# Optimization experiments

Measured on AMD Instinct MI355X. Metric: run time of the kernel, lower is better.

The kernel has to match this reference:

```python
import jax, jax.numpy as jnp
import numpy as np

TEMPERATURE = 1.0
EPS = 1e-12  # matches torch F.normalize eps


def setup_inputs() -> dict:
    key = jax.random.key(0)
    k1, k2 = jax.random.split(key)
    query_features = jax.random.normal(k1, (128, 640, 32, 32), dtype=jnp.float32)
    support_features = jax.random.normal(k2, (5, 640, 32, 32), dtype=jnp.float32)
    return {"query_features": query_features, "support_features": support_features}


def _l2norm(x):
    # F.normalize: x / max(||x||, eps)
    n = jnp.linalg.norm(x, axis=-1, keepdims=True)
    return x / jnp.maximum(n, EPS)


def reference(query_features, support_features):
    NQ, C, H, W = query_features.shape
    # (NQ, C, H, W) -> (NQ, N, C)
    q_patches = query_features.reshape(NQ, C, H * W).transpose(0, 2, 1)
    s_patches = support_features.reshape(support_features.shape[0], C, H * W).transpose(0, 2, 1)
    s_proto = s_patches.mean(axis=0)          # (N, C) prototype over shots
    q_norm = _l2norm(q_patches)               # (NQ, N, C)
    s_norm = _l2norm(s_proto)                 # (N, C)
    sim = jnp.einsum('qnc,mc->qnm', q_norm, s_norm)  # (NQ, N, N)
    max_sim = sim.max(axis=-1)                # (NQ, N) best support patch per query patch
    scores = max_sim.mean(axis=-1) / TEMPERATURE  # (NQ,)
    return scores
```

## Files before the change

### kernel.cpp

```cpp
#include <hip/hip_runtime.h>
#include <stdint.h>


#define NQ   128
#define NP   1024
#define C    640
#define NSH  5
#define EPSN 1e-12f
#define QPITCH 132

typedef __attribute__((ext_vector_type(8))) __bf16 bf16x8;
typedef __attribute__((ext_vector_type(4))) float  f32x4;
typedef __attribute__((ext_vector_type(4))) unsigned int u32x4;

__device__ __forceinline__ unsigned short f2bf(float f) {
  unsigned int u = __builtin_bit_cast(unsigned int, f);
  unsigned int r = (u + 0x7fffu + ((u >> 16) & 1u)) >> 16;
  return (unsigned short)r;
}

__device__ __forceinline__ void gload16(const void* g, void* l) {
  __builtin_amdgcn_global_load_lds(
      (const __attribute__((address_space(1))) void*)g,
      (__attribute__((address_space(3))) void*)l, 16, 0, 0);
}

__global__ __launch_bounds__(256) void prep_s_kernel(
    const float* __restrict__ sup, unsigned short* __restrict__ Sb) {
  __shared__ float red[16][17];
  __shared__ float invn[16];
  int t = threadIdx.x;
  int tm = t & 15, tcg = t >> 4;
  int m = blockIdx.x * 16 + tm;

  float sumsq = 0.f;
  for (int c = tcg; c < C; c += 16) {
    float p = 0.f;
    #pragma unroll
    for (int s = 0; s < NSH; ++s) p += sup[((size_t)s * C + c) * NP + m];
    p *= 0.2f;
    sumsq += p * p;
  }
  red[tcg][tm] = sumsq;
  __syncthreads();
  if (t < 16) {
    float s = 0.f;
    #pragma unroll
    for (int g = 0; g < 16; ++g) s += red[g][t];
    invn[t] = 1.f / fmaxf(sqrtf(s), EPSN);
  }
  __syncthreads();
  float iv = invn[tm];
  for (int c = tcg; c < C; c += 16) {
    float p = 0.f;
    #pragma unroll
    for (int s = 0; s < NSH; ++s) p += sup[((size_t)s * C + c) * NP + m];
    p *= 0.2f;
    Sb[((size_t)(c >> 3) * 1024 + m) * 8 + (c & 7)] = f2bf(p * iv);
  }
}

template <int CC>
__device__ __forceinline__ void q_step(const float* __restrict__ Qbase,
                                       float* __restrict__ qchunk,
                                       f32x4& sq, int nq, int cg, int arow,
                                       int quad,
                                       bf16x8& f00, bf16x8& f01,
                                       bf16x8& f10, bf16x8& f11) {
  #pragma unroll
  for (int i = 0; i < 8; ++i) {
    int c = cg + i * 8;
    f32x4 v = *(const f32x4*)(Qbase + (size_t)(CC * 64 + c) * NP);
    sq += v * v;
    *(f32x4*)&qchunk[c * QPITCH + nq * 4] = v;
  }
  __syncthreads();
  #pragma unroll
  for (int s = 0; s < 2; ++s) {
    #pragma unroll
    for (int nf = 0; nf < 2; ++nf) {
      int row = arow + nf * 16;
      unsigned int uw[4];
      #pragma unroll
      for (int jj = 0; jj < 4; ++jj) {
        int k0 = s * 32 + quad * 8 + jj * 2;
        float v0 = qchunk[k0 * QPITCH + row];
        float v1 = qchunk[(k0 + 1) * QPITCH + row];
        uw[jj] = (unsigned)f2bf(v0) | ((unsigned)f2bf(v1) << 16);
      }
      u32x4 uu = {uw[0], uw[1], uw[2], uw[3]};
      bf16x8 r = __builtin_bit_cast(bf16x8, uu);
      if (s == 0 && nf == 0) f00 = r;
      else if (s == 0 && nf == 1) f01 = r;
      else if (s == 1 && nf == 0) f10 = r;
      else f11 = r;
    }
  }
  __syncthreads();
}

__global__ __launch_bounds__(256, 2) void fused_gemm_kernel(
    const float* __restrict__ Q, const unsigned short* __restrict__ Sb,
    float* __restrict__ partial) {
  __shared__ __align__(16) char Rg[40960];
  __shared__ float invq[128];
  __shared__ float maxbuf[128];
  __shared__ float ssum[2];

  const int t = threadIdx.x;
  const int lane = t & 63, w = t >> 6;
  const int l15 = lane & 15, quad = lane >> 4;
  const int q = blockIdx.x, ns = blockIdx.y;
  const int n0 = ns * 128;

  float* qchunk = (float*)Rg;
  float* qsums  = (float*)(Rg + 33792);
  bf16x8 aF[40];
  const int nq = t & 31, cg = t >> 5;
  const float* Qbase = Q + (size_t)q * C * NP + n0 + nq * 4;
  const int arow = w * 32 + l15;
  f32x4 sq = {0.f, 0.f, 0.f, 0.f};

  q_step<0>(Qbase, qchunk, sq, nq, cg, arow, quad, aF[0],  aF[1],  aF[2],  aF[3]);
  q_step<1>(Qbase, qchunk, sq, nq, cg, arow, quad, aF[4],  aF[5],  aF[6],  aF[7]);
  q_step<2>(Qbase, qchunk, sq, nq, cg, arow, quad, aF[8],  aF[9],  aF[10], aF[11]);
  q_step<3>(Qbase, qchunk, sq, nq, cg, arow, quad, aF[12], aF[13], aF[14], aF[15]);
  q_step<4>(Qbase, qchunk, sq, nq, cg, arow, quad, aF[16], aF[17], aF[18], aF[19]);
  q_step<5>(Qbase, qchunk, sq, nq, cg, arow, quad, aF[20], aF[21], aF[22], aF[23]);
  q_step<6>(Qbase, qchunk, sq, nq, cg, arow, quad, aF[24], aF[25], aF[26], aF[27]);
  q_step<7>(Qbase, qchunk, sq, nq, cg, arow, quad, aF[28], aF[29], aF[30], aF[31]);
  q_step<8>(Qbase, qchunk, sq, nq, cg, arow, quad, aF[32], aF[33], aF[34], aF[35]);
  q_step<9>(Qbase, qchunk, sq, nq, cg, arow, quad, aF[36], aF[37], aF[38], aF[39]);

  #pragma unroll
  for (int j = 0; j < 4; ++j) qsums[cg * 128 + nq * 4 + j] = sq[j];
  __syncthreads();
  if (t < 128) {
    float s = 0.f;
    #pragma unroll
    for (int g = 0; g < 8; ++g) s += qsums[g * 128 + t];
    invq[t] = 1.f / fmaxf(sqrtf(s), EPSN);
  }
  __syncthreads();

  unsigned short* Ss = (unsigned short*)Rg;
  f32x4 ninf = {-3.0e38f, -3.0e38f, -3.0e38f, -3.0e38f};
  f32x4 rm[2] = {ninf, ninf};

  for (int mt = 0; mt < 16; ++mt) {
    f32x4 zero = {0.f, 0.f, 0.f, 0.f};
    f32x4 acc[2][4];
    #pragma unroll
    for (int nf = 0; nf < 2; ++nf)
      #pragma unroll
      for (int mf = 0; mf < 4; ++mf) acc[nf][mf] = zero;

    #pragma unroll
    for (int h = 0; h < 2; ++h) {
      const unsigned short* gsrc =
          Sb + ((size_t)(h * 40 + w) * 1024 + mt * 64 + lane) * 8;
      #pragma unroll
      for (int it = 0; it < 10; ++it)
        gload16(gsrc + (size_t)it * 32768, (char*)Ss + (it * 256 + t) * 16);
      __syncthreads();
      #pragma unroll
      for (int ks = 0; ks < 10; ++ks) {
        #pragma unroll
        for (int mf = 0; mf < 4; ++mf) {
          bf16x8 b = *(const bf16x8*)((char*)Ss +
              (size_t)(((ks * 4 + quad) * 64) + mf * 16 + l15) * 16);
          acc[0][mf] = __builtin_amdgcn_mfma_f32_16x16x32_bf16(
              aF[(h * 10 + ks) * 2 + 0], b, acc[0][mf], 0, 0, 0);
          acc[1][mf] = __builtin_amdgcn_mfma_f32_16x16x32_bf16(
              aF[(h * 10 + ks) * 2 + 1], b, acc[1][mf], 0, 0, 0);
        }
      }
      __syncthreads();
    }
    #pragma unroll
    for (int nf = 0; nf < 2; ++nf)
      #pragma unroll
      for (int r = 0; r < 4; ++r) {
        float mv = fmaxf(fmaxf(acc[nf][0][r], acc[nf][1][r]),
                         fmaxf(acc[nf][2][r], acc[nf][3][r]));
        rm[nf][r] = fmaxf(rm[nf][r], mv);
      }
  }

  #pragma unroll
  for (int off = 8; off >= 1; off >>= 1)
    #pragma unroll
    for (int nf = 0; nf < 2; ++nf)
      #pragma unroll
      for (int r = 0; r < 4; ++r)
        rm[nf][r] = fmaxf(rm[nf][r], __shfl_xor(rm[nf][r], off, 64));
  if (l15 == 0) {
    #pragma unroll
    for (int nf = 0; nf < 2; ++nf)
      #pragma unroll
      for (int r = 0; r < 4; ++r)
        maxbuf[w * 32 + nf * 16 + quad * 4 + r] = rm[nf][r];
  }
  __syncthreads();
  if (t < 128) {
    float v = maxbuf[t] * invq[t];
    #pragma unroll
    for (int off = 32; off >= 1; off >>= 1) v += __shfl_down(v, off, 64);
    if (lane == 0) ssum[w] = v;
  }
  __syncthreads();
  if (t == 0)
    partial[q * 8 + ns] = (ssum[0] + ssum[1]) * (1.f / 1024.f);
}

__global__ void reduce_out_kernel(const float* __restrict__ partial,
                                  float* __restrict__ out) {
  int t = threadIdx.x;
  float s = 0.f;
  #pragma unroll
  for (int i = 0; i < 8; ++i) s += partial[t * 8 + i];
  out[t] = s;
}

extern "C" void kernel_launch(void* const* d_in, const int* in_sizes, int n_in,
                              void* d_out, int out_size, void* d_ws, size_t ws_size,
                              hipStream_t stream) {
  const float* Q = (const float*)d_in[0];
  const float* S = (const float*)d_in[1];
  char* ws = (char*)d_ws;

  unsigned short* Sb   = (unsigned short*)ws;
  float*          part = (float*)(ws + 1310720ull);
  float*          out  = (float*)d_out;

  prep_s_kernel<<<64, 256, 0, stream>>>(S, Sb);
  fused_gemm_kernel<<<dim3(128, 8), 256, 0, stream>>>(Q, Sb, part);
  reduce_out_kernel<<<1, 128, 0, stream>>>(part, out);
}
```

Baseline: 641.4 us.

## Spill tail Q fragments to LDS and parallelize support prep across more blocks

The support-prototype prep is split into three kernels: zero a sum-of-squares buffer, accumulate per-column squared norms with atomics over a 4x20 grid, then normalize and pack to bf16 over a 4x80 grid. This replaces the old 64-block kernel that read the support tensor twice with little parallelism. In the main GEMM, the last 8 of 40 register-resident A fragments are stored in a padded LDS buffer and read back during the MFMA loop. This cuts VGPR pressure so the kernel can be pinned at two waves per EU, at the cost of extra LDS reads and extra LDS use per block.

```diff
diff --git a/kernel.cpp b/kernel.cpp
--- a/kernel.cpp
+++ b/kernel.cpp
@@ -8,6 +8,7 @@
 #define NSH  5
 #define EPSN 1e-12f
 #define QPITCH 132
+#define QAPITCH 130
 
 typedef __attribute__((ext_vector_type(8))) __bf16 bf16x8;
 typedef __attribute__((ext_vector_type(4))) float  f32x4;
@@ -25,44 +26,55 @@
       (__attribute__((address_space(3))) void*)l, 16, 0, 0);
 }
 
-__global__ __launch_bounds__(256) void prep_s_kernel(
-    const float* __restrict__ sup, unsigned short* __restrict__ Sb) {
-  __shared__ float red[16][17];
-  __shared__ float invn[16];
-  int t = threadIdx.x;
-  int tm = t & 15, tcg = t >> 4;
-  int m = blockIdx.x * 16 + tm;
-
-  float sumsq = 0.f;
-  for (int c = tcg; c < C; c += 16) {
+__global__ __launch_bounds__(256) void zero_ssq_kernel(float* __restrict__ ssq) {
+  ssq[blockIdx.x * 256 + threadIdx.x] = 0.f;
+}
+
+__global__ __launch_bounds__(256) void prep_sa_kernel(
+    const float* __restrict__ sup, float* __restrict__ ssq) {
+  const int t = threadIdx.x;
+  const int m = blockIdx.x * 256 + t;
+  const int c0 = blockIdx.y * 32;
+  float ps = 0.f;
+  #pragma unroll 4
+  for (int c = c0; c < c0 + 32; ++c) {
     float p = 0.f;
     #pragma unroll
     for (int s = 0; s < NSH; ++s) p += sup[((size_t)s * C + c) * NP + m];
     p *= 0.2f;
-    sumsq += p * p;
-  }
-  red[tcg][tm] = sumsq;
-  __syncthreads();
-  if (t < 16) {
-    float s = 0.f;
-    #pragma unroll
-    for (int g = 0; g < 16; ++g) s += red[g][t];
-    invn[t] = 1.f / fmaxf(sqrtf(s), EPSN);
-  }
-  __syncthreads();
-  float iv = invn[tm];
-  for (int c = tcg; c < C; c += 16) {
-    float p = 0.f;
-    #pragma unroll
-    for (int s = 0; s < NSH; ++s) p += sup[((size_t)s * C + c) * NP + m];
-    p *= 0.2f;
-    Sb[((size_t)(c >> 3) * 1024 + m) * 8 + (c & 7)] = f2bf(p * iv);
-  }
-}
-
-template <int CC>
+    ps += p * p;
+  }
+  atomicAdd(&ssq[m], ps);
+}
+
+__global__ __launch_bounds__(256) void prep_sb_kernel(
+    const float* __restrict__ sup, const float* __restrict__ ssq,
+    unsigned short* __restrict__ Sb) {
+  const int t = threadIdx.x;
+  const int m = blockIdx.x * 256 + t;
+  const int k4 = blockIdx.y;
+  const int c0 = k4 * 8;
+  const float iv = 1.f / fmaxf(sqrtf(ssq[m]), EPSN);
+  unsigned int uw[4];
+  #pragma unroll
+  for (int j = 0; j < 4; ++j) {
+    float p0 = 0.f, p1 = 0.f;
+    #pragma unroll
+    for (int s = 0; s < NSH; ++s) {
+      p0 += sup[((size_t)s * C + c0 + 2 * j) * NP + m];
+      p1 += sup[((size_t)s * C + c0 + 2 * j + 1) * NP + m];
+    }
+    p0 *= 0.2f; p1 *= 0.2f;
+    uw[j] = (unsigned)f2bf(p0 * iv) | ((unsigned)f2bf(p1 * iv) << 16);
+  }
+  u32x4 uu = {uw[0], uw[1], uw[2], uw[3]};
+  *(u32x4*)&Sb[((size_t)k4 * NP + m) * 8] = uu;
+}
+
+template <int CC, bool TAIL>
 __device__ __forceinline__ void q_step(const float* __restrict__ Qbase,
                                        float* __restrict__ qchunk,
+                                       unsigned short* __restrict__ Qa,
                                        f32x4& sq, int nq, int cg, int arow,
                                        int quad,
                                        bf16x8& f00, bf16x8& f01,
@@ -89,20 +101,28 @@
         uw[jj] = (unsigned)f2bf(v0) | ((unsigned)f2bf(v1) << 16);
       }
       u32x4 uu = {uw[0], uw[1], uw[2], uw[3]};
-      bf16x8 r = __builtin_bit_cast(bf16x8, uu);
-      if (s == 0 && nf == 0) f00 = r;
-      else if (s == 0 && nf == 1) f01 = r;
-      else if (s == 1 && nf == 0) f10 = r;
-      else f11 = r;
+      if constexpr (TAIL) {
+        int slab = (CC - 8) * 8 + s * 4 + quad;
+        *(u32x4*)&Qa[(size_t)(slab * QAPITCH + row) * 8] = uu;
+      } else {
+        bf16x8 r = __builtin_bit_cast(bf16x8, uu);
+        if (s == 0 && nf == 0) f00 = r;
+        else if (s == 0 && nf == 1) f01 = r;
+        else if (s == 1 && nf == 0) f10 = r;
+        else f11 = r;
+      }
     }
   }
   __syncthreads();
 }
 
-__global__ __launch_bounds__(256, 2) void fused_gemm_kernel(
+__global__ __launch_bounds__(256)
+__attribute__((amdgpu_waves_per_eu(2, 2)))
+void fused_gemm_kernel(
     const float* __restrict__ Q, const unsigned short* __restrict__ Sb,
     float* __restrict__ partial) {
   __shared__ __align__(16) char Rg[40960];
+  __shared__ __align__(16) unsigned short Qa[16 * QAPITCH * 8];
   __shared__ float invq[128];
   __shared__ float maxbuf[128];
   __shared__ float ssum[2];
@@ -115,22 +135,23 @@
 
   float* qchunk = (float*)Rg;
   float* qsums  = (float*)(Rg + 33792);
-  bf16x8 aF[40];
+  bf16x8 aF[32];
+  bf16x8 dm;
   const int nq = t & 31, cg = t >> 5;
   const float* Qbase = Q + (size_t)q * C * NP + n0 + nq * 4;
   const int arow = w * 32 + l15;
   f32x4 sq = {0.f, 0.f, 0.f, 0.f};
 
-  q_step<0>(Qbase, qchunk, sq, nq, cg, arow, quad, aF[0],  aF[1],  aF[2],  aF[3]);
-  q_step<1>(Qbase, qchunk, sq, nq, cg, arow, quad, aF[4],  aF[5],  aF[6],  aF[7]);
-  q_step<2>(Qbase, qchunk, sq, nq, cg, arow, quad, aF[8],  aF[9],  aF[10], aF[11]);
-  q_step<3>(Qbase, qchunk, sq, nq, cg, arow, quad, aF[12], aF[13], aF[14], aF[15]);
-  q_step<4>(Qbase, qchunk, sq, nq, cg, arow, quad, aF[16], aF[17], aF[18], aF[19]);
-  q_step<5>(Qbase, qchunk, sq, nq, cg, arow, quad, aF[20], aF[21], aF[22], aF[23]);
-  q_step<6>(Qbase, qchunk, sq, nq, cg, arow, quad, aF[24], aF[25], aF[26], aF[27]);
-  q_step<7>(Qbase, qchunk, sq, nq, cg, arow, quad, aF[28], aF[29], aF[30], aF[31]);
-  q_step<8>(Qbase, qchunk, sq, nq, cg, arow, quad, aF[32], aF[33], aF[34], aF[35]);
-  q_step<9>(Qbase, qchunk, sq, nq, cg, arow, quad, aF[36], aF[37], aF[38], aF[39]);
+  q_step<0, false>(Qbase, qchunk, Qa, sq, nq, cg, arow, quad, aF[0],  aF[1],  aF[2],  aF[3]);
+  q_step<1, false>(Qbase, qchunk, Qa, sq, nq, cg, arow, quad, aF[4],  aF[5],  aF[6],  aF[7]);
+  q_step<2, false>(Qbase, qchunk, Qa, sq, nq, cg, arow, quad, aF[8],  aF[9],  aF[10], aF[11]);
+  q_step<3, false>(Qbase, qchunk, Qa, sq, nq, cg, arow, quad, aF[12], aF[13], aF[14], aF[15]);
+  q_step<4, false>(Qbase, qchunk, Qa, sq, nq, cg, arow, quad, aF[16], aF[17], aF[18], aF[19]);
+  q_step<5, false>(Qbase, qchunk, Qa, sq, nq, cg, arow, quad, aF[20], aF[21], aF[22], aF[23]);
+  q_step<6, false>(Qbase, qchunk, Qa, sq, nq, cg, arow, quad, aF[24], aF[25], aF[26], aF[27]);
+  q_step<7, false>(Qbase, qchunk, Qa, sq, nq, cg, arow, quad, aF[28], aF[29], aF[30], aF[31]);
+  q_step<8, true >(Qbase, qchunk, Qa, sq, nq, cg, arow, quad, dm, dm, dm, dm);
+  q_step<9, true >(Qbase, qchunk, Qa, sq, nq, cg, arow, quad, dm, dm, dm, dm);
 
   #pragma unroll
   for (int j = 0; j < 4; ++j) qsums[cg * 128 + nq * 4 + j] = sq[j];
@@ -165,14 +186,24 @@
       __syncthreads();
       #pragma unroll
       for (int ks = 0; ks < 10; ++ks) {
+        const int gks = h * 10 + ks;
+        bf16x8 a0, a1;
+        if (gks < 16) {
+          a0 = aF[(gks & 15) * 2 + 0];
+          a1 = aF[(gks & 15) * 2 + 1];
+        } else {
+          const int slab = ((gks - 16) & 3) * 4 + quad;
+          a0 = *(const bf16x8*)&Qa[(size_t)(slab * QAPITCH + arow) * 8];
+          a1 = *(const bf16x8*)&Qa[(size_t)(slab * QAPITCH + arow + 16) * 8];
+        }
         #pragma unroll
         for (int mf = 0; mf < 4; ++mf) {
           bf16x8 b = *(const bf16x8*)((char*)Ss +
               (size_t)(((ks * 4 + quad) * 64) + mf * 16 + l15) * 16);
           acc[0][mf] = __builtin_amdgcn_mfma_f32_16x16x32_bf16(
-              aF[(h * 10 + ks) * 2 + 0], b, acc[0][mf], 0, 0, 0);
+              a0, b, acc[0][mf], 0, 0, 0);
           acc[1][mf] = __builtin_amdgcn_mfma_f32_16x16x32_bf16(
-              aF[(h * 10 + ks) * 2 + 1], b, acc[1][mf], 0, 0, 0);
+              a1, b, acc[1][mf], 0, 0, 0);
         }
       }
       __syncthreads();
@@ -231,9 +262,12 @@
 
   unsigned short* Sb   = (unsigned short*)ws;
   float*          part = (float*)(ws + 1310720ull);
+  float*          ssq  = (float*)(ws + 1314816ull);
   float*          out  = (float*)d_out;
 
-  prep_s_kernel<<<64, 256, 0, stream>>>(S, Sb);
+  zero_ssq_kernel<<<4, 256, 0, stream>>>(ssq);
+  prep_sa_kernel<<<dim3(4, 20), 256, 0, stream>>>(S, ssq);
+  prep_sb_kernel<<<dim3(4, 80), 256, 0, stream>>>(S, ssq, Sb);
   fused_gemm_kernel<<<dim3(128, 8), 256, 0, stream>>>(Q, Sb, part);
   reduce_out_kernel<<<1, 128, 0, stream>>>(part, out);
 }
```

Measured after the change: 650.1 us. No clear change (+1.4%).
